# Kernel tuning notes

Hardware: AMD Instinct MI355X
Metric: run time of the kernel (lower is better)

## Reference

```python
import jax, jax.numpy as jnp
import numpy as np

N_HEADS = 16
HEAD_DIM = 64
ROPE_BASE = 10000.0


def _rope_cos_sin(T, d, dtype):
    # GPT-NeoX style: inv_freq over even indices, cos/sin duplicated to full head_dim
    inv_freq = 1.0 / (ROPE_BASE ** (jnp.arange(0, d, 2, dtype=jnp.float32) / d))
    freqs = jnp.arange(T, dtype=jnp.float32)[:, None] * inv_freq[None, :]  # [T, d/2]
    emb = jnp.concatenate([freqs, freqs], axis=-1)  # [T, d]
    return jnp.cos(emb).astype(dtype), jnp.sin(emb).astype(dtype)


def _rotate_half(x):
    x1, x2 = jnp.split(x, 2, axis=-1)
    return jnp.concatenate([-x2, x1], axis=-1)


def setup_inputs() -> dict:
    key = jax.random.key(0)
    k1, k2, k3 = jax.random.split(key, 3)
    B, T, C = 2, 2048, 1024
    x = jax.random.normal(k1, (B, T, C), dtype=jnp.float32)
    Wqkv = jax.random.normal(k2, (C, 3 * C), dtype=jnp.float32) * (1.0 / np.sqrt(C))
    Wout = jax.random.normal(k3, (C, C), dtype=jnp.float32) * (1.0 / np.sqrt(C))
    return {"x": x, "Wqkv": Wqkv, "Wout": Wout}


def reference(x, Wqkv, Wout):
    B, T, C = x.shape
    H, D = N_HEADS, HEAD_DIM
    qkv = (x @ Wqkv).reshape(B, T, 3, H, D)
    q, k, v = qkv[:, :, 0], qkv[:, :, 1], qkv[:, :, 2]  # [B,T,H,D]
    q = q.transpose(0, 2, 1, 3)  # [B,H,T,D]
    k = k.transpose(0, 2, 1, 3)
    v = v.transpose(0, 2, 1, 3)
    cos, sin = _rope_cos_sin(T, D, x.dtype)  # [T,D]
    cos = cos[None, None]
    sin = sin[None, None]
    q = q * cos + _rotate_half(q) * sin
    k = k * cos + _rotate_half(k) * sin
    scale = 1.0 / np.sqrt(D)
    scores = jnp.einsum("bhqd,bhkd->bhqk", q, k) * scale  # [B,H,T,T]
    causal = jnp.tril(jnp.ones((T, T), dtype=bool))
    scores = jnp.where(causal[None, None], scores, jnp.finfo(scores.dtype).min)
    attn = jax.nn.softmax(scores, axis=-1)
    out = jnp.einsum("bhqk,bhkd->bhqd", attn, v)  # [B,H,T,D]
    out = out.transpose(0, 2, 1, 3).reshape(B, T, C)
    return out @ Wout
```

## Files before the change

kernel.cpp:

```cpp
#include <hip/hip_runtime.h>


#define B_  2
#define T_  2048
#define C_  1024
#define H_  16
#define D_  64
#define N3_ 3072

typedef unsigned short ushortx8 __attribute__((ext_vector_type(8)));
typedef unsigned short ushortx4 __attribute__((ext_vector_type(4)));
typedef short bf16x8 __attribute__((ext_vector_type(8)));
typedef float f32x4 __attribute__((ext_vector_type(4)));
typedef float f32x16 __attribute__((ext_vector_type(16)));
typedef unsigned int uintx2 __attribute__((ext_vector_type(2)));

__device__ __forceinline__ unsigned short f2bf(float f) {
  union { float f; unsigned u; } v; v.f = f;
  unsigned r = v.u + 0x7FFFu + ((v.u >> 16) & 1u);
  return (unsigned short)(r >> 16);
}
__device__ __forceinline__ float bf2f(unsigned short h) {
  union { unsigned u; float f; } v; v.u = ((unsigned)h) << 16;
  return v.f;
}
__device__ __forceinline__ unsigned cvtpk_bf16(float lo, float hi) {
  unsigned r; asm("v_cvt_pk_bf16_f32 %0, %1, %2" : "=v"(r) : "v"(lo), "v"(hi));
  return r;
}
__device__ __forceinline__ void gload_lds16(const void* g, void* l) {
  __builtin_amdgcn_global_load_lds((const __attribute__((address_space(1))) void*)g,
                                   (__attribute__((address_space(3))) void*)l,
                                   16, 0, 0);
}

__global__ __launch_bounds__(256) void cvt_x_kernel(const float* __restrict__ x,
                                                    unsigned short* __restrict__ xb) {
  size_t i = ((size_t)blockIdx.x * 256 + threadIdx.x) * 4;
  const float4 v = *(const float4*)(x + i);
  ushortx4 o;
  o[0] = f2bf(v.x); o[1] = f2bf(v.y); o[2] = f2bf(v.z); o[3] = f2bf(v.w);
  *(ushortx4*)(xb + i) = o;
}

__global__ __launch_bounds__(256) void tconv_kernel(const float* __restrict__ W,
                                                    unsigned short* __restrict__ WT,
                                                    int K, int N) {
  __shared__ float tile[32][33];
  const int n0 = blockIdx.x * 32, k0 = blockIdx.y * 32;
  const int tx = threadIdx.x & 31, ty = threadIdx.x >> 5;
#pragma unroll
  for (int i = 0; i < 4; ++i)
    tile[ty + i * 8][tx] = W[(size_t)(k0 + ty + i * 8) * N + n0 + tx];
  __syncthreads();
#pragma unroll
  for (int i = 0; i < 4; ++i)
    WT[(size_t)(n0 + ty + i * 8) * K + k0 + tx] = f2bf(tile[tx][ty + i * 8]);
}

__global__ __launch_bounds__(512, 2) void gemm256_kernel(const unsigned short* __restrict__ A,
                                                         const unsigned short* __restrict__ BT,
                                                         unsigned short* __restrict__ Cb,
                                                         int M, int N, int K) {
  __shared__ unsigned short Alds[2][256 * 64];
  __shared__ unsigned short Blds[2][256 * 64];
  const int tid = threadIdx.x, w = tid >> 6, l = tid & 63;
  const int wm = w >> 2, wn = w & 3;
  const int lg = l >> 4, lr = l & 15;
  const int lr8 = l >> 3, lc8 = (l & 7) ^ lr8;
  const int bid = blockIdx.x;
  const int swz = (bid & 7) * 24 + (bid >> 3);
  const int nbn = N >> 8;
  const int bm = swz / nbn, bn = swz % nbn;
  const int m0 = bm * 256, n0 = bn * 256;
  const int NT = K >> 6;

  f32x4 acc[8][4];
#pragma unroll
  for (int i = 0; i < 8; ++i)
#pragma unroll
    for (int j = 0; j < 4; ++j) acc[i][j] = f32x4{0.f, 0.f, 0.f, 0.f};

  auto stage2 = [&](int b, int k0n, int ph) {
    const int ca = w * 4 + ph;
    gload_lds16(A + (size_t)(m0 + ca * 8 + lr8) * K + k0n + lc8 * 8, &Alds[b][ca * 512]);
    gload_lds16(BT + (size_t)(n0 + ca * 8 + lr8) * K + k0n + lc8 * 8, &Blds[b][ca * 512]);
  };
#pragma unroll
  for (int ph = 0; ph < 4; ++ph) stage2(0, 0, ph);

  for (int kt = 0; kt < NT; ++kt) {
    const int buf = kt & 1;
    const unsigned short* AL = &Alds[buf][0];
    const unsigned short* BL = &Blds[buf][0];
    const int k0n = (kt + 1) * 64;
    const bool more = (kt + 1 < NT);
    if (more) {
      stage2(buf ^ 1, k0n, 0);
      asm volatile("s_waitcnt vmcnt(2)" ::: "memory");
    } else {
      asm volatile("s_waitcnt vmcnt(0)" ::: "memory");
    }
    __builtin_amdgcn_s_barrier();
    __builtin_amdgcn_sched_barrier(0);
    bf16x8 bfr[4][2];
#pragma unroll
    for (int nj = 0; nj < 4; ++nj)
#pragma unroll
      for (int kc = 0; kc < 2; ++kc) {
        const int row = wn * 64 + nj * 16 + lr;
        bfr[nj][kc] = *(const bf16x8*)(&BL[row * 64 + (((kc * 4 + lg) ^ (row & 7))) * 8]);
      }
#pragma unroll
    for (int q = 0; q < 4; ++q) {
      if (q > 0 && more) stage2(buf ^ 1, k0n, q);
      bf16x8 afp[2][2];
#pragma unroll
      for (int mi2 = 0; mi2 < 2; ++mi2)
#pragma unroll
        for (int kc = 0; kc < 2; ++kc) {
          const int row = wm * 128 + (q * 2 + mi2) * 16 + lr;
          afp[mi2][kc] = *(const bf16x8*)(&AL[row * 64 + (((kc * 4 + lg) ^ (row & 7))) * 8]);
        }
      __builtin_amdgcn_s_setprio(1);
#pragma unroll
      for (int mi2 = 0; mi2 < 2; ++mi2)
#pragma unroll
        for (int nj = 0; nj < 4; ++nj)
#pragma unroll
          for (int kc = 0; kc < 2; ++kc)
            acc[q * 2 + mi2][nj] = __builtin_amdgcn_mfma_f32_16x16x32_bf16(
                afp[mi2][kc], bfr[nj][kc], acc[q * 2 + mi2][nj], 0, 0, 0);
      __builtin_amdgcn_s_setprio(0);
    }
    __builtin_amdgcn_s_barrier();
  }
#pragma unroll
  for (int mi = 0; mi < 8; ++mi)
#pragma unroll
    for (int nj = 0; nj < 4; ++nj)
#pragma unroll
      for (int j = 0; j < 4; ++j) {
        const int row = m0 + wm * 128 + mi * 16 + lg * 4 + j;
        const int col = n0 + wn * 64 + nj * 16 + lr;
        Cb[(size_t)row * N + col] = f2bf(acc[mi][nj][j]);
      }
}

template <int OUTF32>
__global__ __launch_bounds__(256) void gemm_bt_kernel(const unsigned short* __restrict__ A,
                                                      const unsigned short* __restrict__ BT,
                                                      void* __restrict__ Cptr,
                                                      int M, int N, int K) {
  __shared__ unsigned short Alds[128 * 64];
  __shared__ unsigned short Blds[128 * 64];
  const int tid = threadIdx.x;
  const int w = tid >> 6, l = tid & 63;
  const int wr = w >> 1, wc = w & 1;
  const int lg = l >> 4, lr = l & 15;
  const int m0 = blockIdx.y * 128, n0 = blockIdx.x * 128;
  const int lr8 = l >> 3;
  const int lc8 = (l & 7) ^ lr8;

  f32x4 acc[4][4];
#pragma unroll
  for (int i = 0; i < 4; ++i)
#pragma unroll
    for (int j = 0; j < 4; ++j) acc[i][j] = f32x4{0.f, 0.f, 0.f, 0.f};

  for (int k0 = 0; k0 < K; k0 += 64) {
    __syncthreads();
#pragma unroll
    for (int i = 0; i < 4; ++i) {
      const int ch = w * 4 + i;
      gload_lds16(A + (size_t)(m0 + ch * 8 + lr8) * K + k0 + lc8 * 8, &Alds[ch * 512]);
      gload_lds16(BT + (size_t)(n0 + ch * 8 + lr8) * K + k0 + lc8 * 8, &Blds[ch * 512]);
    }
    __syncthreads();
#pragma unroll
    for (int kc = 0; kc < 2; ++kc) {
      bf16x8 af[4], bfr[4];
#pragma unroll
      for (int mi = 0; mi < 4; ++mi) {
        const int row = wr * 64 + mi * 16 + lr;
        const int c16 = (kc * 4 + lg) ^ (row & 7);
        af[mi] = *(const bf16x8*)(&Alds[row * 64 + c16 * 8]);
      }
#pragma unroll
      for (int nj = 0; nj < 4; ++nj) {
        const int row = wc * 64 + nj * 16 + lr;
        const int c16 = (kc * 4 + lg) ^ (row & 7);
        bfr[nj] = *(const bf16x8*)(&Blds[row * 64 + c16 * 8]);
      }
#pragma unroll
      for (int mi = 0; mi < 4; ++mi)
#pragma unroll
        for (int nj = 0; nj < 4; ++nj)
          acc[mi][nj] = __builtin_amdgcn_mfma_f32_16x16x32_bf16(af[mi], bfr[nj], acc[mi][nj], 0, 0, 0);
    }
  }
#pragma unroll
  for (int mi = 0; mi < 4; ++mi)
#pragma unroll
    for (int nj = 0; nj < 4; ++nj)
#pragma unroll
      for (int j = 0; j < 4; ++j) {
        const int row = m0 + wr * 64 + mi * 16 + lg * 4 + j;
        const int col = n0 + wc * 64 + nj * 16 + lr;
        if (OUTF32) ((float*)Cptr)[(size_t)row * N + col] = acc[mi][nj][j];
        else ((unsigned short*)Cptr)[(size_t)row * N + col] = f2bf(acc[mi][nj][j]);
      }
}

__global__ __launch_bounds__(256) void rope_pack_kernel(const unsigned short* __restrict__ QKV,
                                                        unsigned short* __restrict__ Qp,
                                                        unsigned short* __restrict__ Kp) {
  const int tt = blockIdx.x, bh = blockIdx.y;
  const int b = bh >> 4, h = bh & 15;
  const int tid = threadIdx.x;
  const int half = tid >> 7;
  const int r = (tid >> 1) & 63;
  const int d0 = (tid & 1) * 16;
  const int t = tt * 64 + r;
  const unsigned short* src = QKV + (size_t)(b * T_ + t) * N3_ + half * C_ + h * D_;
  ushortx8 lo0 = *(const ushortx8*)(src + d0);
  ushortx8 lo1 = *(const ushortx8*)(src + d0 + 8);
  ushortx8 hi0 = *(const ushortx8*)(src + d0 + 32);
  ushortx8 hi1 = *(const ushortx8*)(src + d0 + 40);
  ushortx8 olo0, olo1, ohi0, ohi1;
  const float scale = half ? 1.0f : 0.18033688011112042f;
  const float tf = (float)t;
#pragma unroll
  for (int jj = 0; jj < 16; ++jj) {
    const int d = d0 + jj;
    const float invf = exp2f((float)d * -0.41524101186092036f);
    const float ang = tf * invf;
    const float c = cosf(ang), s = sinf(ang);
    const float xl = bf2f(jj < 8 ? lo0[jj] : lo1[jj - 8]);
    const float xh = bf2f(jj < 8 ? hi0[jj] : hi1[jj - 8]);
    const unsigned short rl = f2bf((xl * c - xh * s) * scale);
    const unsigned short rh = f2bf((xh * c + xl * s) * scale);
    if (jj < 8) { olo0[jj] = rl; ohi0[jj] = rh; }
    else        { olo1[jj - 8] = rl; ohi1[jj - 8] = rh; }
  }
  unsigned short* dst = (half ? Kp : Qp) + ((size_t)bh * T_ + t) * D_;
  *(ushortx8*)(dst + d0) = olo0;
  *(ushortx8*)(dst + d0 + 8) = olo1;
  *(ushortx8*)(dst + d0 + 32) = ohi0;
  *(ushortx8*)(dst + d0 + 40) = ohi1;
}

__global__ __launch_bounds__(256) void vtrans_kernel(const unsigned short* __restrict__ QKV,
                                                     unsigned short* __restrict__ Vt) {
  __shared__ unsigned short tile[64][72];
  const int tt = blockIdx.x, bh = blockIdx.y;
  const int b = bh >> 4, h = bh & 15;
  const int tid = threadIdx.x;
  {
    const int r = tid >> 2, seg = tid & 3;
    const unsigned short* src = QKV + (size_t)(b * T_ + tt * 64 + r) * N3_ + 2 * C_ + h * D_ + seg * 16;
    *(ushortx8*)(&tile[r][seg * 16]) = *(const ushortx8*)(src);
    *(ushortx8*)(&tile[r][seg * 16 + 8]) = *(const ushortx8*)(src + 8);
  }
  __syncthreads();
  {
    const int d = tid >> 2, ts = tid & 3;
    ushortx8 o0, o1;
#pragma unroll
    for (int i = 0; i < 8; ++i) { o0[i] = tile[ts * 16 + i][d]; o1[i] = tile[ts * 16 + 8 + i][d]; }
    unsigned short* dst = Vt + ((size_t)bh * D_ + d) * T_ + tt * 64 + ts * 16;
    *(ushortx8*)(dst) = o0;
    *(ushortx8*)(dst + 8) = o1;
  }
}

__global__ __launch_bounds__(256, 2) void attn7_kernel(const unsigned short* __restrict__ Qp,
                                                       const unsigned short* __restrict__ Kp,
                                                       const unsigned short* __restrict__ Vt,
                                                       unsigned short* __restrict__ Ob) {
  __shared__ unsigned short Klds[3][64 * 64];
  __shared__ unsigned short Vlds[3][64 * 64];
  const int tid = threadIdx.x, w = tid >> 6, l = tid & 63;
  const int lq = l & 31, hi = l >> 5;
  const int swz = lq & 7;
  const int bid = blockIdx.x;
  const int bh = bid & 31;
  const int pp = bid >> 5;
  const int p = (pp < 8) ? pp : 23 - pp;
  const int s = (w < 2) ? (2 * p + w) : (62 - 2 * p + (w - 2));
  const int q0 = s * 32;
  const int ntiles = 32 - p;
  const size_t koff = (size_t)bh * T_ * D_;
  const unsigned short* Kb = Kp + koff;
  const unsigned short* Vb = Vt + (size_t)bh * D_ * T_;

  const int lr8 = l >> 3;
  const int lc8 = (l & 7) ^ lr8;

  bf16x8 qf[4];
  {
    const unsigned short* qp = Qp + koff + (size_t)(q0 + lq) * D_ + hi * 8;
#pragma unroll
    for (int ds = 0; ds < 4; ++ds) qf[ds] = *(const bf16x8*)(qp + ds * 16);
  }
  f32x16 o0, o1;
#pragma unroll
  for (int r = 0; r < 16; ++r) { o0[r] = 0.f; o1[r] = 0.f; }
  float m = -3.0e38f, lden = 0.f;

#pragma unroll
  for (int i = 0; i < 2; ++i) {
    const int c = w * 2 + i;
    gload_lds16(Kb + (size_t)(c * 8 + lr8) * D_ + lc8 * 8, &Klds[0][c * 512]);
    gload_lds16(Vb + (size_t)(c * 8 + lr8) * T_ + lc8 * 8, &Vlds[0][c * 512]);
  }

  for (int kt = 0; kt < ntiles; ++kt) {
    const int cur = kt % 3;
    const int nxt = (kt + 1) % 3;
    const int ktn = (kt + 1 < ntiles) ? kt + 1 : kt;
    const int kvn = ktn * 64;
#pragma unroll
    for (int i = 0; i < 2; ++i) {
      const int c = w * 2 + i;
      gload_lds16(Kb + (size_t)(kvn + c * 8 + lr8) * D_ + lc8 * 8, &Klds[nxt][c * 512]);
      gload_lds16(Vb + (size_t)(c * 8 + lr8) * T_ + kvn + lc8 * 8, &Vlds[nxt][c * 512]);
    }
    asm volatile("s_waitcnt vmcnt(4)" ::: "memory");
    __builtin_amdgcn_s_barrier();
    __builtin_amdgcn_sched_barrier(0);

    const int kv0 = kt * 64;
    if (kv0 <= q0 + 31) {
      const unsigned short* KL = &Klds[cur][0];
      const unsigned short* VL = &Vlds[cur][0];
      f32x16 acc0, acc1;
#pragma unroll
      for (int r = 0; r < 16; ++r) { acc0[r] = 0.f; acc1[r] = 0.f; }
      __builtin_amdgcn_s_setprio(1);
#pragma unroll
      for (int ds = 0; ds < 4; ++ds) {
        const int slot = ((ds * 2 + hi) ^ swz) * 8;
        const bf16x8 kf0 = *(const bf16x8*)(&KL[(lq) * 64 + slot]);
        const bf16x8 kf1 = *(const bf16x8*)(&KL[(32 + lq) * 64 + slot]);
        acc0 = __builtin_amdgcn_mfma_f32_32x32x16_bf16(kf0, qf[ds], acc0, 0, 0, 0);
        acc1 = __builtin_amdgcn_mfma_f32_32x32x16_bf16(kf1, qf[ds], acc1, 0, 0, 0);
      }
      __builtin_amdgcn_s_setprio(0);
      if (kv0 + 63 > q0) {
        const int thr0 = q0 + lq - kv0;
        const int thr1 = thr0 - 32;
#pragma unroll
        for (int r = 0; r < 16; ++r) {
          const int kvloc = (r & 3) + 8 * (r >> 2) + 4 * hi;
          if (kvloc > thr0) acc0[r] = -3.0e38f;
          if (kvloc > thr1) acc1[r] = -3.0e38f;
        }
      }
      float mx[8];
#pragma unroll
      for (int i = 0; i < 8; ++i)
        mx[i] = fmaxf(fmaxf(acc0[i], acc0[i + 8]), fmaxf(acc1[i], acc1[i + 8]));
#pragma unroll
      for (int i = 0; i < 4; ++i) mx[i] = fmaxf(mx[i], mx[i + 4]);
      const float mloc = fmaxf(fmaxf(mx[0], mx[1]), fmaxf(mx[2], mx[3]));
      const uintx2 mp = __builtin_amdgcn_permlane32_swap(__float_as_uint(mloc), __float_as_uint(mloc), false, false);
      const float pm = fmaxf(__uint_as_float(mp.x), __uint_as_float(mp.y));
      const bool grow = pm > m + 8.0f;
      if (__any(grow)) {
        const float mn = grow ? pm : m;
        const float alpha = __builtin_amdgcn_exp2f(m - mn);
        m = mn;
        lden *= alpha;
#pragma unroll
        for (int r = 0; r < 16; ++r) { o0[r] *= alpha; o1[r] *= alpha; }
      }
      float p0[16], p1[16];
#pragma unroll
      for (int r = 0; r < 16; ++r) {
        p0[r] = __builtin_amdgcn_exp2f(acc0[r] - m);
        p1[r] = __builtin_amdgcn_exp2f(acc1[r] - m);
      }
      unsigned W0 = cvtpk_bf16(p0[0], p0[1]), W1 = cvtpk_bf16(p0[2], p0[3]);
      unsigned W2 = cvtpk_bf16(p0[4], p0[5]), W3 = cvtpk_bf16(p0[6], p0[7]);
      uintx2 Aa = __builtin_amdgcn_permlane32_swap(W0, W2, false, false);
      uintx2 Ab = __builtin_amdgcn_permlane32_swap(W1, W3, false, false);
      union { unsigned u[4]; bf16x8 v; } pfa0 = {{Aa.x, Ab.x, Aa.y, Ab.y}};
      W0 = cvtpk_bf16(p0[8], p0[9]);   W1 = cvtpk_bf16(p0[10], p0[11]);
      W2 = cvtpk_bf16(p0[12], p0[13]); W3 = cvtpk_bf16(p0[14], p0[15]);
      Aa = __builtin_amdgcn_permlane32_swap(W0, W2, false, false);
      Ab = __builtin_amdgcn_permlane32_swap(W1, W3, false, false);
      union { unsigned u[4]; bf16x8 v; } pfa1 = {{Aa.x, Ab.x, Aa.y, Ab.y}};
      W0 = cvtpk_bf16(p1[0], p1[1]);   W1 = cvtpk_bf16(p1[2], p1[3]);
      W2 = cvtpk_bf16(p1[4], p1[5]);   W3 = cvtpk_bf16(p1[6], p1[7]);
      Aa = __builtin_amdgcn_permlane32_swap(W0, W2, false, false);
      Ab = __builtin_amdgcn_permlane32_swap(W1, W3, false, false);
      union { unsigned u[4]; bf16x8 v; } pfb0 = {{Aa.x, Ab.x, Aa.y, Ab.y}};
      W0 = cvtpk_bf16(p1[8], p1[9]);   W1 = cvtpk_bf16(p1[10], p1[11]);
      W2 = cvtpk_bf16(p1[12], p1[13]); W3 = cvtpk_bf16(p1[14], p1[15]);
      Aa = __builtin_amdgcn_permlane32_swap(W0, W2, false, false);
      Ab = __builtin_amdgcn_permlane32_swap(W1, W3, false, false);
      union { unsigned u[4]; bf16x8 v; } pfb1 = {{Aa.x, Ab.x, Aa.y, Ab.y}};

      __builtin_amdgcn_s_setprio(1);
#pragma unroll
      for (int dt = 0; dt < 2; ++dt) {
        const int rowb = (dt * 32 + lq) * 64;
        const bf16x8 vf0 = *(const bf16x8*)(&VL[rowb + ((0 * 2 + hi) ^ swz) * 8]);
        const bf16x8 vf1 = *(const bf16x8*)(&VL[rowb + ((1 * 2 + hi) ^ swz) * 8]);
        const bf16x8 vf2 = *(const bf16x8*)(&VL[rowb + ((2 * 2 + hi) ^ swz) * 8]);
        const bf16x8 vf3 = *(const bf16x8*)(&VL[rowb + ((3 * 2 + hi) ^ swz) * 8]);
        if (dt == 0) {
          o0 = __builtin_amdgcn_mfma_f32_32x32x16_bf16(vf0, pfa0.v, o0, 0, 0, 0);
          o0 = __builtin_amdgcn_mfma_f32_32x32x16_bf16(vf1, pfa1.v, o0, 0, 0, 0);
          o0 = __builtin_amdgcn_mfma_f32_32x32x16_bf16(vf2, pfb0.v, o0, 0, 0, 0);
          o0 = __builtin_amdgcn_mfma_f32_32x32x16_bf16(vf3, pfb1.v, o0, 0, 0, 0);
        } else {
          o1 = __builtin_amdgcn_mfma_f32_32x32x16_bf16(vf0, pfa0.v, o1, 0, 0, 0);
          o1 = __builtin_amdgcn_mfma_f32_32x32x16_bf16(vf1, pfa1.v, o1, 0, 0, 0);
          o1 = __builtin_amdgcn_mfma_f32_32x32x16_bf16(vf2, pfb0.v, o1, 0, 0, 0);
          o1 = __builtin_amdgcn_mfma_f32_32x32x16_bf16(vf3, pfb1.v, o1, 0, 0, 0);
        }
      }
      __builtin_amdgcn_s_setprio(0);
      float sm[8];
#pragma unroll
      for (int i = 0; i < 8; ++i) sm[i] = (p0[i] + p0[i + 8]) + (p1[i] + p1[i + 8]);
#pragma unroll
      for (int i = 0; i < 4; ++i) sm[i] = sm[i] + sm[i + 4];
      const float sloc = (sm[0] + sm[1]) + (sm[2] + sm[3]);
      const uintx2 sp = __builtin_amdgcn_permlane32_swap(__float_as_uint(sloc), __float_as_uint(sloc), false, false);
      lden += __uint_as_float(sp.x) + __uint_as_float(sp.y);
    }
  }
  asm volatile("s_waitcnt vmcnt(0)" ::: "memory");

  const float rl = __builtin_amdgcn_rcpf(lden);
  const int b = bh >> 4, hh = bh & 15;
  unsigned short* orow = Ob + (size_t)(b * T_ + q0 + lq) * C_ + hh * D_ + 4 * hi;
#pragma unroll
  for (int rq = 0; rq < 4; ++rq) {
    ushortx4 ov0, ov1;
#pragma unroll
    for (int i = 0; i < 4; ++i) {
      ov0[i] = f2bf(o0[rq * 4 + i] * rl);
      ov1[i] = f2bf(o1[rq * 4 + i] * rl);
    }
    *(ushortx4*)(orow + rq * 8) = ov0;
    *(ushortx4*)(orow + 32 + rq * 8) = ov1;
  }
}

extern "C" void kernel_launch(void* const* d_in, const int* in_sizes, int n_in,
                              void* d_out, int out_size, void* d_ws, size_t ws_size,
                              hipStream_t stream) {
  const float* x = (const float*)d_in[0];
  const float* Wqkv = (const float*)d_in[1];
  const float* Wout = (const float*)d_in[2];
  float* out = (float*)d_out;
  char* ws = (char*)d_ws;
  unsigned short* Xb    = (unsigned short*)(ws);
  unsigned short* WqkvT = (unsigned short*)(ws + (8ull << 20));
  unsigned short* WoutT = (unsigned short*)(ws + (14ull << 20));
  unsigned short* QKVb  = (unsigned short*)(ws + (16ull << 20));
  unsigned short* Qp    = (unsigned short*)(ws + (40ull << 20));
  unsigned short* Kp    = (unsigned short*)(ws + (48ull << 20));
  unsigned short* Vt    = (unsigned short*)(ws + (56ull << 20));
  unsigned short* Ob    = (unsigned short*)(ws + (64ull << 20));

  cvt_x_kernel<<<4096, 256, 0, stream>>>(x, Xb);
  tconv_kernel<<<dim3(N3_ / 32, C_ / 32), 256, 0, stream>>>(Wqkv, WqkvT, C_, N3_);
  tconv_kernel<<<dim3(C_ / 32, C_ / 32), 256, 0, stream>>>(Wout, WoutT, C_, C_);
  gemm256_kernel<<<(B_ * T_ / 256) * (N3_ / 256), 512, 0, stream>>>(
      Xb, WqkvT, QKVb, B_ * T_, N3_, C_);
  rope_pack_kernel<<<dim3(T_ / 64, B_ * H_), 256, 0, stream>>>(QKVb, Qp, Kp);
  vtrans_kernel<<<dim3(T_ / 64, B_ * H_), 256, 0, stream>>>(QKVb, Vt);
  attn7_kernel<<<512, 256, 0, stream>>>(Qp, Kp, Vt, Ob);
  gemm_bt_kernel<1><<<dim3(C_ / 128, (B_ * T_) / 128), 256, 0, stream>>>(
      Ob, WoutT, out, B_ * T_, C_, C_);
}
```

Before: 139.3 us.

## Split GEMM LDS tiles into k-halves with finer-grained staged pipeline

Reorganizes the 256x256 bf16 GEMM's shared-memory tiles into separate 32-wide k-chunks for A and B. Loads are issued in four phases per k-step, and each phase uses its own vmcnt wait, barrier and MFMA group, so the next tile's copy overlaps the current compute more finely. The launch bound drops to 1 block per CU, which frees registers but reduces occupancy. The design also adds more barriers per iteration, and the vmcnt counts are tuned by hand, which makes correctness fragile.

```diff
diff --git a/kernel.cpp b/kernel.cpp
--- a/kernel.cpp
+++ b/kernel.cpp
@@ -58,20 +58,20 @@
     WT[(size_t)(n0 + ty + i * 8) * K + k0 + tx] = f2bf(tile[tx][ty + i * 8]);
 }
 
-__global__ __launch_bounds__(512, 2) void gemm256_kernel(const unsigned short* __restrict__ A,
+__global__ __launch_bounds__(512, 1) void gemm256_kernel(const unsigned short* __restrict__ A,
                                                          const unsigned short* __restrict__ BT,
                                                          unsigned short* __restrict__ Cb,
                                                          int M, int N, int K) {
-  __shared__ unsigned short Alds[2][256 * 64];
-  __shared__ unsigned short Blds[2][256 * 64];
+  __shared__ unsigned short Akl[2][2][256 * 32];
+  __shared__ unsigned short Bkl[2][2][256 * 32];
   const int tid = threadIdx.x, w = tid >> 6, l = tid & 63;
   const int wm = w >> 2, wn = w & 3;
   const int lg = l >> 4, lr = l & 15;
-  const int lr8 = l >> 3, lc8 = (l & 7) ^ lr8;
+  const int ric = l >> 2, sl = l & 3;
   const int bid = blockIdx.x;
-  const int swz = (bid & 7) * 24 + (bid >> 3);
+  const int swzb = (bid & 7) * 24 + (bid >> 3);
   const int nbn = N >> 8;
-  const int bm = swz / nbn, bn = swz % nbn;
+  const int bm = swzb / nbn, bn = swzb % nbn;
   const int m0 = bm * 256, n0 = bn * 256;
   const int NT = K >> 6;
 
@@ -81,59 +81,64 @@
 #pragma unroll
     for (int j = 0; j < 4; ++j) acc[i][j] = f32x4{0.f, 0.f, 0.f, 0.f};
 
-  auto stage2 = [&](int b, int k0n, int ph) {
-    const int ca = w * 4 + ph;
-    gload_lds16(A + (size_t)(m0 + ca * 8 + lr8) * K + k0n + lc8 * 8, &Alds[b][ca * 512]);
-    gload_lds16(BT + (size_t)(n0 + ca * 8 + lr8) * K + k0n + lc8 * 8, &Blds[b][ca * 512]);
+  auto stageH = [&](int d, int side, int kch, int k0) {
+#pragma unroll
+    for (int j = 0; j < 2; ++j) {
+      const int ch = w + 8 * j;
+      const int r = ch * 16 + ric;
+      const int cs = sl ^ (r & 3);
+      if (side == 0)
+        gload_lds16(A + (size_t)(m0 + r) * K + k0 + kch * 32 + cs * 8, &Akl[d][kch][ch * 512]);
+      else
+        gload_lds16(BT + (size_t)(n0 + r) * K + k0 + kch * 32 + cs * 8, &Bkl[d][kch][ch * 512]);
+    }
   };
-#pragma unroll
-  for (int ph = 0; ph < 4; ++ph) stage2(0, 0, ph);
+
+  stageH(0, 0, 0, 0); stageH(0, 1, 0, 0); stageH(0, 0, 1, 0); stageH(0, 1, 1, 0);
 
   for (int kt = 0; kt < NT; ++kt) {
-    const int buf = kt & 1;
-    const unsigned short* AL = &Alds[buf][0];
-    const unsigned short* BL = &Blds[buf][0];
-    const int k0n = (kt + 1) * 64;
+    const int d = kt & 1, nd = d ^ 1;
+    const int k1 = (kt + 1) * 64;
     const bool more = (kt + 1 < NT);
-    if (more) {
-      stage2(buf ^ 1, k0n, 0);
-      asm volatile("s_waitcnt vmcnt(2)" ::: "memory");
-    } else {
-      asm volatile("s_waitcnt vmcnt(0)" ::: "memory");
-    }
-    __builtin_amdgcn_s_barrier();
-    __builtin_amdgcn_sched_barrier(0);
-    bf16x8 bfr[4][2];
-#pragma unroll
-    for (int nj = 0; nj < 4; ++nj)
-#pragma unroll
-      for (int kc = 0; kc < 2; ++kc) {
-        const int row = wn * 64 + nj * 16 + lr;
-        bfr[nj][kc] = *(const bf16x8*)(&BL[row * 64 + (((kc * 4 + lg) ^ (row & 7))) * 8]);
-      }
-#pragma unroll
-    for (int q = 0; q < 4; ++q) {
-      if (q > 0 && more) stage2(buf ^ 1, k0n, q);
-      bf16x8 afp[2][2];
-#pragma unroll
-      for (int mi2 = 0; mi2 < 2; ++mi2)
-#pragma unroll
-        for (int kc = 0; kc < 2; ++kc) {
-          const int row = wm * 128 + (q * 2 + mi2) * 16 + lr;
-          afp[mi2][kc] = *(const bf16x8*)(&AL[row * 64 + (((kc * 4 + lg) ^ (row & 7))) * 8]);
+    bf16x8 bfr[4];
+#pragma unroll
+    for (int ph = 0; ph < 4; ++ph) {
+      const int kc = ph >> 1;
+      const int mh = ph & 1;
+      if (more) stageH(nd, ph & 1, ph >> 1, k1);
+      if (ph == 0) {
+        if (more) asm volatile("s_waitcnt vmcnt(6)" ::: "memory");
+        else      asm volatile("s_waitcnt vmcnt(4)" ::: "memory");
+      } else if (ph == 2) {
+        if (more) asm volatile("s_waitcnt vmcnt(6)" ::: "memory");
+        else      asm volatile("s_waitcnt vmcnt(0)" ::: "memory");
+      }
+      __builtin_amdgcn_s_barrier();
+      asm volatile("" ::: "memory");
+      if (mh == 0) {
+#pragma unroll
+        for (int nj = 0; nj < 4; ++nj) {
+          const int r = wn * 64 + nj * 16 + lr;
+          bfr[nj] = *(const bf16x8*)(&Bkl[d][kc][r * 32 + (lg ^ (r & 3)) * 8]);
         }
+      }
+      bf16x8 af[4];
+#pragma unroll
+      for (int i = 0; i < 4; ++i) {
+        const int r = wm * 128 + (mh * 4 + i) * 16 + lr;
+        af[i] = *(const bf16x8*)(&Akl[d][kc][r * 32 + (lg ^ (r & 3)) * 8]);
+      }
       __builtin_amdgcn_s_setprio(1);
 #pragma unroll
-      for (int mi2 = 0; mi2 < 2; ++mi2)
+      for (int i = 0; i < 4; ++i)
 #pragma unroll
         for (int nj = 0; nj < 4; ++nj)
-#pragma unroll
-          for (int kc = 0; kc < 2; ++kc)
-            acc[q * 2 + mi2][nj] = __builtin_amdgcn_mfma_f32_16x16x32_bf16(
-                afp[mi2][kc], bfr[nj][kc], acc[q * 2 + mi2][nj], 0, 0, 0);
+          acc[mh * 4 + i][nj] = __builtin_amdgcn_mfma_f32_16x16x32_bf16(
+              af[i], bfr[nj], acc[mh * 4 + i][nj], 0, 0, 0);
       __builtin_amdgcn_s_setprio(0);
-    }
-    __builtin_amdgcn_s_barrier();
+      asm volatile("" ::: "memory");
+      __builtin_amdgcn_s_barrier();
+    }
   }
 #pragma unroll
   for (int mi = 0; mi < 8; ++mi)
```

Result: no change. 139.7 us (+0.3%).
